# Optimization experiments

Hardware: AMD Instinct MI355X
Metric: run time of the kernel (lower is better)

## Reference

```python
import jax, jax.numpy as jnp
import numpy as np

B, T, C, N = 2, 2048, 4096, 4096

def setup_inputs() -> dict:
    key = jax.random.key(0)
    k1, k2, k3, k4 = jax.random.split(key, 4)
    y = jax.random.normal(k1, (B, T, C), dtype=jnp.float32)
    # quantized weight: uint8 codes in [0,255], stored/used as float after upcast
    weight = jnp.round(jax.random.uniform(k2, (C, N), dtype=jnp.float32) * 255.0)
    rng = jax.random.uniform(k3, (1, 1, C), dtype=jnp.float32) * 0.01  # per-input-channel scale
    offset = jax.random.normal(k4, (C,), dtype=jnp.float32) * 0.01    # per-input-channel offset
    return {"y": y, "weight": weight, "rng": rng, "offset": offset}

def reference(y, weight, rng, offset):
    # yv = y.reshape(-1,C) @ offset -> [B,T,1] correction term
    yv = jnp.einsum('btc,c->bt', y, offset)[..., None]
    # (y * range) @ weight  (dequantized GEMM) + correction
    out = jnp.einsum('btc,cn->btn', y * rng, weight) + yv
    return out
```

## Files before the change

### kernel.cpp

```cpp
#include <hip/hip_runtime.h>

typedef unsigned short u16;
typedef unsigned int u32;
typedef unsigned char u8;
typedef signed char i8;

typedef int i32x4 __attribute__((ext_vector_type(4)));

__global__ __launch_bounds__(256) void quant_y_kernel(const float* __restrict__ y,
                                                      const float* __restrict__ rng,
                                                      const float* __restrict__ off,
                                                      uint4* __restrict__ qy,
                                                      float* __restrict__ sp,
                                                      float* __restrict__ tv) {
    const int row = blockIdx.x;
    const int tid = threadIdx.x;
    const float* yr = y + (size_t)row * 4096;
    const int base = tid * 16;

    float ysr[16];
    float amax = 0.0f, s1 = 0.0f, s2 = 0.0f;
    #pragma unroll
    for (int ii = 0; ii < 4; ++ii) {
        float4 v = *(const float4*)&yr[base + ii * 4];
        float4 g = *(const float4*)&rng[base + ii * 4];
        float4 o = *(const float4*)&off[base + ii * 4];
        float p0 = v.x * g.x, p1 = v.y * g.y, p2 = v.z * g.z, p3 = v.w * g.w;
        ysr[ii * 4 + 0] = p0; ysr[ii * 4 + 1] = p1;
        ysr[ii * 4 + 2] = p2; ysr[ii * 4 + 3] = p3;
        s1 += p0 + p1 + p2 + p3;
        s2 += v.x * o.x + v.y * o.y + v.z * o.z + v.w * o.w;
        amax = fmaxf(amax, fmaxf(fmaxf(fabsf(p0), fabsf(p1)), fmaxf(fabsf(p2), fabsf(p3))));
    }
    #pragma unroll
    for (int d = 32; d > 0; d >>= 1) {
        amax = fmaxf(amax, __shfl_down(amax, d));
        s1 += __shfl_down(s1, d);
        s2 += __shfl_down(s2, d);
    }
    __shared__ float ra[4], rs1[4], rs2[4];
    const int wv = tid >> 6;
    if ((tid & 63) == 0) { ra[wv] = amax; rs1[wv] = s1; rs2[wv] = s2; }
    __syncthreads();
    const float sm = fmaxf(fmaxf(ra[0], ra[1]), fmaxf(ra[2], ra[3]));
    const float inv = sm > 0.0f ? 127.0f / sm : 0.0f;

    u32 d[4];
    #pragma unroll
    for (int g = 0; g < 4; ++g) {
        u32 b0 = (u8)(i8)(int)rintf(ysr[g * 4 + 0] * inv);
        u32 b1 = (u8)(i8)(int)rintf(ysr[g * 4 + 1] * inv);
        u32 b2 = (u8)(i8)(int)rintf(ysr[g * 4 + 2] * inv);
        u32 b3 = (u8)(i8)(int)rintf(ysr[g * 4 + 3] * inv);
        d[g] = b0 | (b1 << 8) | (b2 << 16) | (b3 << 24);
    }
    const int j = (tid & 7) ^ (row & 7);
    qy[(size_t)row * 256 + (tid >> 3) * 8 + j] = make_uint4(d[0], d[1], d[2], d[3]);
    if (tid == 0) {
        sp[row] = sm / 127.0f;
        tv[row] = 128.0f * (rs1[0] + rs1[1] + rs1[2] + rs1[3])
                        + (rs2[0] + rs2[1] + rs2[2] + rs2[3]);
    }
}

__global__ __launch_bounds__(256) void quant_w_kernel(const float* __restrict__ w,
                                                      uint4* __restrict__ wq) {
    __shared__ i8 tile[64][68];
    const int n0 = (blockIdx.x & 63) * 64;
    const int k0 = (blockIdx.x >> 6) * 64;
    const int c4 = threadIdx.x & 15;
    const int r0 = threadIdx.x >> 4;
    #pragma unroll
    for (int i = 0; i < 4; ++i) {
        int kk = r0 + i * 16;
        float4 v = *(const float4*)&w[(size_t)(k0 + kk) * 4096 + n0 + c4 * 4];
        u32 b0 = (u8)(i8)((int)v.x - 128);
        u32 b1 = (u8)(i8)((int)v.y - 128);
        u32 b2 = (u8)(i8)((int)v.z - 128);
        u32 b3 = (u8)(i8)((int)v.w - 128);
        *(u32*)&tile[kk][c4 * 4] = b0 | (b1 << 8) | (b2 << 16) | (b3 << 24);
    }
    __syncthreads();
    const int nl = threadIdx.x >> 2;
    const int ci = threadIdx.x & 3;
    const int l = ((k0 >> 4) & 7) + ci;
    const int j = l ^ ((n0 + nl) & 7);
    u32 d[4];
    #pragma unroll
    for (int g = 0; g < 4; ++g) {
        int kl = ci * 16 + g * 4;
        d[g] = (u32)(u8)tile[kl + 0][nl] | ((u32)(u8)tile[kl + 1][nl] << 8)
             | ((u32)(u8)tile[kl + 2][nl] << 16) | ((u32)(u8)tile[kl + 3][nl] << 24);
    }
    wq[(size_t)(n0 + nl) * 256 + (k0 >> 7) * 8 + j] = make_uint4(d[0], d[1], d[2], d[3]);
}

__device__ inline void gld16(const i8* g, i8* l) {
    __builtin_amdgcn_global_load_lds((const __attribute__((address_space(1))) void*)g,
                                     (__attribute__((address_space(3))) void*)l,
                                     16, 0, 0);
}

__global__ __launch_bounds__(256) void gemm_kernel(const i8* __restrict__ qy,
                                                   const i8* __restrict__ wq,
                                                   const float* __restrict__ sp,
                                                   const float* __restrict__ tv,
                                                   float* __restrict__ out) {
    __shared__ i8 As[128 * 128];
    __shared__ i8 Bs[128 * 128];
    const int bid = blockIdx.x;
    const int xcd = bid & 7;
    const int jj = bid >> 3;
    const int bn = (xcd * 4 + (jj & 3)) * 128;
    const int bm = (jj >> 2) * 128;

    const int lane = threadIdx.x & 63;
    const int wv = threadIdx.x >> 6;
    const int wm = (wv >> 1) * 64;
    const int wn = (wv & 1) * 64;
    const int r = lane & 15;
    const int q = lane >> 4;
    const int j0 = q ^ (r & 7);

    const int rsub = lane >> 3;
    const int jsub = lane & 7;
    const i8* gA[4]; const i8* gB[4]; i8* lA[4]; i8* lB[4];
    #pragma unroll
    for (int c = 0; c < 4; ++c) {
        int ca = wv * 4 + c;
        gA[c] = qy + (size_t)(bm + ca * 8 + rsub) * 4096 + jsub * 16;
        gB[c] = wq + (size_t)(bn + ca * 8 + rsub) * 4096 + jsub * 16;
        lA[c] = &As[ca * 1024];
        lB[c] = &Bs[ca * 1024];
    }

    i32x4 acc[4][4] = {};

    for (int kt = 0; kt < 32; ++kt) {
        #pragma unroll
        for (int c = 0; c < 4; ++c) {
            gld16(gA[c], lA[c]);
            gld16(gB[c], lB[c]);
            gA[c] += 128; gB[c] += 128;
        }
        __syncthreads();

        #pragma unroll
        for (int s = 0; s < 2; ++s) {
            const int js = (j0 ^ (s * 4)) * 16;
            i32x4 af[4], bfr[4];
            #pragma unroll
            for (int i = 0; i < 4; ++i)
                af[i] = *(const i32x4*)&As[(wm + i * 16 + r) * 128 + js];
            #pragma unroll
            for (int i = 0; i < 4; ++i)
                bfr[i] = *(const i32x4*)&Bs[(wn + i * 16 + r) * 128 + js];
            #pragma unroll
            for (int i = 0; i < 4; ++i) {
                #pragma unroll
                for (int j = 0; j < 4; ++j)
                    acc[i][j] = __builtin_amdgcn_mfma_i32_16x16x64_i8(af[i], bfr[j], acc[i][j], 0, 0, 0);
            }
        }
        __syncthreads();
    }

    #pragma unroll
    for (int i = 0; i < 4; ++i) {
        #pragma unroll
        for (int rr = 0; rr < 4; ++rr) {
            const int gm = bm + wm + i * 16 + q * 4 + rr;
            const float sc = sp[gm];
            const float tt = tv[gm];
            #pragma unroll
            for (int j = 0; j < 4; ++j) {
                const int gn = bn + wn + j * 16 + r;
                out[(size_t)gm * 4096 + gn] = sc * (float)acc[i][j][rr] + tt;
            }
        }
    }
}

extern "C" void kernel_launch(void* const* d_in, const int* in_sizes, int n_in,
                              void* d_out, int out_size, void* d_ws, size_t ws_size,
                              hipStream_t stream) {
    const float* y   = (const float*)d_in[0];
    const float* w   = (const float*)d_in[1];
    const float* rng = (const float*)d_in[2];
    const float* off = (const float*)d_in[3];
    float* out = (float*)d_out;

    i8* qy = (i8*)d_ws;
    i8* wq = qy + (size_t)4096 * 4096;
    float* sp = (float*)(wq + (size_t)4096 * 4096);
    float* tv = sp + 4096;

    quant_y_kernel<<<4096, 256, 0, stream>>>(y, rng, off, (uint4*)qy, sp, tv);
    quant_w_kernel<<<4096, 256, 0, stream>>>(w, (uint4*)wq);
    gemm_kernel<<<1024, 256, 0, stream>>>(qy, wq, sp, tv, out);
}
```

Baseline: 246.7 us.

## Fuse quant kernels and use double-buffered 256x256 int8 GEMM tiles

Merges the activation and weight quantization kernels into one launch with a branch on block index. The GEMM moves to 256x256 block tiles with 8 waves, each computing 128x64. LDS is double-buffered so the next K tile's global-to-LDS loads are issued during the current tile's MFMAs, with barriers interleaved and s_setprio raised around MFMA bursts. This aims to hide load latency and raise reuse per byte, at the cost of 128KB of LDS per block and only 256 blocks, which may leave some CUs idle.

```diff
diff --git a/kernel.cpp b/kernel.cpp
--- a/kernel.cpp
+++ b/kernel.cpp
@@ -7,175 +7,235 @@
 
 typedef int i32x4 __attribute__((ext_vector_type(4)));
 
-__global__ __launch_bounds__(256) void quant_y_kernel(const float* __restrict__ y,
-                                                      const float* __restrict__ rng,
-                                                      const float* __restrict__ off,
-                                                      uint4* __restrict__ qy,
-                                                      float* __restrict__ sp,
-                                                      float* __restrict__ tv) {
-    const int row = blockIdx.x;
-    const int tid = threadIdx.x;
-    const float* yr = y + (size_t)row * 4096;
-    const int base = tid * 16;
-
-    float ysr[16];
-    float amax = 0.0f, s1 = 0.0f, s2 = 0.0f;
-    #pragma unroll
-    for (int ii = 0; ii < 4; ++ii) {
-        float4 v = *(const float4*)&yr[base + ii * 4];
-        float4 g = *(const float4*)&rng[base + ii * 4];
-        float4 o = *(const float4*)&off[base + ii * 4];
-        float p0 = v.x * g.x, p1 = v.y * g.y, p2 = v.z * g.z, p3 = v.w * g.w;
-        ysr[ii * 4 + 0] = p0; ysr[ii * 4 + 1] = p1;
-        ysr[ii * 4 + 2] = p2; ysr[ii * 4 + 3] = p3;
-        s1 += p0 + p1 + p2 + p3;
-        s2 += v.x * o.x + v.y * o.y + v.z * o.z + v.w * o.w;
-        amax = fmaxf(amax, fmaxf(fmaxf(fabsf(p0), fabsf(p1)), fmaxf(fabsf(p2), fabsf(p3))));
-    }
-    #pragma unroll
-    for (int d = 32; d > 0; d >>= 1) {
-        amax = fmaxf(amax, __shfl_down(amax, d));
-        s1 += __shfl_down(s1, d);
-        s2 += __shfl_down(s2, d);
-    }
-    __shared__ float ra[4], rs1[4], rs2[4];
-    const int wv = tid >> 6;
-    if ((tid & 63) == 0) { ra[wv] = amax; rs1[wv] = s1; rs2[wv] = s2; }
-    __syncthreads();
-    const float sm = fmaxf(fmaxf(ra[0], ra[1]), fmaxf(ra[2], ra[3]));
-    const float inv = sm > 0.0f ? 127.0f / sm : 0.0f;
-
-    u32 d[4];
-    #pragma unroll
-    for (int g = 0; g < 4; ++g) {
-        u32 b0 = (u8)(i8)(int)rintf(ysr[g * 4 + 0] * inv);
-        u32 b1 = (u8)(i8)(int)rintf(ysr[g * 4 + 1] * inv);
-        u32 b2 = (u8)(i8)(int)rintf(ysr[g * 4 + 2] * inv);
-        u32 b3 = (u8)(i8)(int)rintf(ysr[g * 4 + 3] * inv);
-        d[g] = b0 | (b1 << 8) | (b2 << 16) | (b3 << 24);
-    }
-    const int j = (tid & 7) ^ (row & 7);
-    qy[(size_t)row * 256 + (tid >> 3) * 8 + j] = make_uint4(d[0], d[1], d[2], d[3]);
-    if (tid == 0) {
-        sp[row] = sm / 127.0f;
-        tv[row] = 128.0f * (rs1[0] + rs1[1] + rs1[2] + rs1[3])
-                        + (rs2[0] + rs2[1] + rs2[2] + rs2[3]);
-    }
-}
-
-__global__ __launch_bounds__(256) void quant_w_kernel(const float* __restrict__ w,
-                                                      uint4* __restrict__ wq) {
-    __shared__ i8 tile[64][68];
-    const int n0 = (blockIdx.x & 63) * 64;
-    const int k0 = (blockIdx.x >> 6) * 64;
-    const int c4 = threadIdx.x & 15;
-    const int r0 = threadIdx.x >> 4;
-    #pragma unroll
-    for (int i = 0; i < 4; ++i) {
-        int kk = r0 + i * 16;
-        float4 v = *(const float4*)&w[(size_t)(k0 + kk) * 4096 + n0 + c4 * 4];
-        u32 b0 = (u8)(i8)((int)v.x - 128);
-        u32 b1 = (u8)(i8)((int)v.y - 128);
-        u32 b2 = (u8)(i8)((int)v.z - 128);
-        u32 b3 = (u8)(i8)((int)v.w - 128);
-        *(u32*)&tile[kk][c4 * 4] = b0 | (b1 << 8) | (b2 << 16) | (b3 << 24);
-    }
-    __syncthreads();
-    const int nl = threadIdx.x >> 2;
-    const int ci = threadIdx.x & 3;
-    const int l = ((k0 >> 4) & 7) + ci;
-    const int j = l ^ ((n0 + nl) & 7);
-    u32 d[4];
-    #pragma unroll
-    for (int g = 0; g < 4; ++g) {
-        int kl = ci * 16 + g * 4;
-        d[g] = (u32)(u8)tile[kl + 0][nl] | ((u32)(u8)tile[kl + 1][nl] << 8)
-             | ((u32)(u8)tile[kl + 2][nl] << 16) | ((u32)(u8)tile[kl + 3][nl] << 24);
-    }
-    wq[(size_t)(n0 + nl) * 256 + (k0 >> 7) * 8 + j] = make_uint4(d[0], d[1], d[2], d[3]);
-}
-
 __device__ inline void gld16(const i8* g, i8* l) {
     __builtin_amdgcn_global_load_lds((const __attribute__((address_space(1))) void*)g,
                                      (__attribute__((address_space(3))) void*)l,
                                      16, 0, 0);
 }
 
-__global__ __launch_bounds__(256) void gemm_kernel(const i8* __restrict__ qy,
-                                                   const i8* __restrict__ wq,
-                                                   const float* __restrict__ sp,
-                                                   const float* __restrict__ tv,
-                                                   float* __restrict__ out) {
-    __shared__ i8 As[128 * 128];
-    __shared__ i8 Bs[128 * 128];
+__global__ __launch_bounds__(256) void prep_kernel(const float* __restrict__ y,
+                                                   const float* __restrict__ rng,
+                                                   const float* __restrict__ off,
+                                                   const float* __restrict__ w,
+                                                   uint4* __restrict__ qy,
+                                                   uint4* __restrict__ wq,
+                                                   float* __restrict__ sp,
+                                                   float* __restrict__ tv) {
+    __shared__ i8 tile[64][68];
+    __shared__ float ra[4], rs1[4], rs2[4];
+    const int tid = threadIdx.x;
+
+    if (blockIdx.x < 4096) {
+        const int row = blockIdx.x;
+        const float* yr = y + (size_t)row * 4096;
+        const int base = tid * 16;
+
+        float ysr[16];
+        float amax = 0.0f, s1 = 0.0f, s2 = 0.0f;
+        #pragma unroll
+        for (int ii = 0; ii < 4; ++ii) {
+            float4 v = *(const float4*)&yr[base + ii * 4];
+            float4 g = *(const float4*)&rng[base + ii * 4];
+            float4 o = *(const float4*)&off[base + ii * 4];
+            float p0 = v.x * g.x, p1 = v.y * g.y, p2 = v.z * g.z, p3 = v.w * g.w;
+            ysr[ii * 4 + 0] = p0; ysr[ii * 4 + 1] = p1;
+            ysr[ii * 4 + 2] = p2; ysr[ii * 4 + 3] = p3;
+            s1 += p0 + p1 + p2 + p3;
+            s2 += v.x * o.x + v.y * o.y + v.z * o.z + v.w * o.w;
+            amax = fmaxf(amax, fmaxf(fmaxf(fabsf(p0), fabsf(p1)), fmaxf(fabsf(p2), fabsf(p3))));
+        }
+        #pragma unroll
+        for (int d = 32; d > 0; d >>= 1) {
+            amax = fmaxf(amax, __shfl_down(amax, d));
+            s1 += __shfl_down(s1, d);
+            s2 += __shfl_down(s2, d);
+        }
+        const int wv = tid >> 6;
+        if ((tid & 63) == 0) { ra[wv] = amax; rs1[wv] = s1; rs2[wv] = s2; }
+        __syncthreads();
+        const float sm = fmaxf(fmaxf(ra[0], ra[1]), fmaxf(ra[2], ra[3]));
+        const float inv = sm > 0.0f ? 127.0f / sm : 0.0f;
+
+        u32 d[4];
+        #pragma unroll
+        for (int g = 0; g < 4; ++g) {
+            u32 b0 = (u8)(i8)(int)rintf(ysr[g * 4 + 0] * inv);
+            u32 b1 = (u8)(i8)(int)rintf(ysr[g * 4 + 1] * inv);
+            u32 b2 = (u8)(i8)(int)rintf(ysr[g * 4 + 2] * inv);
+            u32 b3 = (u8)(i8)(int)rintf(ysr[g * 4 + 3] * inv);
+            d[g] = b0 | (b1 << 8) | (b2 << 16) | (b3 << 24);
+        }
+        const int j = (tid & 7) ^ (row & 7);
+        qy[(size_t)row * 256 + (tid >> 3) * 8 + j] = make_uint4(d[0], d[1], d[2], d[3]);
+        if (tid == 0) {
+            sp[row] = sm / 127.0f;
+            tv[row] = 128.0f * (rs1[0] + rs1[1] + rs1[2] + rs1[3])
+                            + (rs2[0] + rs2[1] + rs2[2] + rs2[3]);
+        }
+    } else {
+        const int bid = blockIdx.x - 4096;
+        const int n0 = (bid & 63) * 64;
+        const int k0 = (bid >> 6) * 64;
+        const int c4 = tid & 15;
+        const int r0 = tid >> 4;
+        #pragma unroll
+        for (int i = 0; i < 4; ++i) {
+            int kk = r0 + i * 16;
+            float4 v = *(const float4*)&w[(size_t)(k0 + kk) * 4096 + n0 + c4 * 4];
+            u32 b0 = (u8)(i8)((int)v.x - 128);
+            u32 b1 = (u8)(i8)((int)v.y - 128);
+            u32 b2 = (u8)(i8)((int)v.z - 128);
+            u32 b3 = (u8)(i8)((int)v.w - 128);
+            *(u32*)&tile[kk][c4 * 4] = b0 | (b1 << 8) | (b2 << 16) | (b3 << 24);
+        }
+        __syncthreads();
+        const int nl = tid >> 2;
+        const int ci = tid & 3;
+        const int l = ((k0 >> 4) & 7) + ci;
+        const int j = l ^ ((n0 + nl) & 7);
+        u32 d[4];
+        #pragma unroll
+        for (int g = 0; g < 4; ++g) {
+            int kl = ci * 16 + g * 4;
+            d[g] = (u32)(u8)tile[kl + 0][nl] | ((u32)(u8)tile[kl + 1][nl] << 8)
+                 | ((u32)(u8)tile[kl + 2][nl] << 16) | ((u32)(u8)tile[kl + 3][nl] << 24);
+        }
+        wq[(size_t)(n0 + nl) * 256 + (k0 >> 7) * 8 + j] = make_uint4(d[0], d[1], d[2], d[3]);
+    }
+}
+
+__global__ __launch_bounds__(512, 2) void gemm_kernel(const i8* __restrict__ qy,
+                                                      const i8* __restrict__ wq,
+                                                      const float* __restrict__ sp,
+                                                      const float* __restrict__ tv,
+                                                      float* __restrict__ out) {
+    __shared__ i8 As[2][256 * 128];
+    __shared__ i8 Bs[2][256 * 128];
+
     const int bid = blockIdx.x;
     const int xcd = bid & 7;
     const int jj = bid >> 3;
-    const int bn = (xcd * 4 + (jj & 3)) * 128;
-    const int bm = (jj >> 2) * 128;
-
-    const int lane = threadIdx.x & 63;
-    const int wv = threadIdx.x >> 6;
-    const int wm = (wv >> 1) * 64;
-    const int wn = (wv & 1) * 64;
+    const int bn = (xcd * 2 + (jj & 1)) * 256;
+    const int bm = (jj >> 1) * 256;
+
+    const int tid = (int)threadIdx.x;
+    const int lane = tid & 63;
+    const int wv = tid >> 6;
+    const int wm = (wv >> 2) * 128;
+    const int wn = (wv & 3) * 64;
     const int r = lane & 15;
     const int q = lane >> 4;
-    const int j0 = q ^ (r & 7);
+    const int col0 = (q ^ (r & 7)) << 4;
+
+    const int offA0 = (wm + r) * 128 + col0;
+    const int offB0 = (wn + r) * 128 + col0;
+    const int offA1 = offA0 ^ 64;
+    const int offB1 = offB0 ^ 64;
 
     const int rsub = lane >> 3;
     const int jsub = lane & 7;
-    const i8* gA[4]; const i8* gB[4]; i8* lA[4]; i8* lB[4];
+    const i8* gA[4]; const i8* gB[4];
+    int ldso[4];
     #pragma unroll
     for (int c = 0; c < 4; ++c) {
-        int ca = wv * 4 + c;
+        const int ca = wv * 4 + c;
         gA[c] = qy + (size_t)(bm + ca * 8 + rsub) * 4096 + jsub * 16;
         gB[c] = wq + (size_t)(bn + ca * 8 + rsub) * 4096 + jsub * 16;
-        lA[c] = &As[ca * 1024];
-        lB[c] = &Bs[ca * 1024];
-    }
-
-    i32x4 acc[4][4] = {};
-
-    for (int kt = 0; kt < 32; ++kt) {
-        #pragma unroll
-        for (int c = 0; c < 4; ++c) {
-            gld16(gA[c], lA[c]);
-            gld16(gB[c], lB[c]);
-            gA[c] += 128; gB[c] += 128;
-        }
-        __syncthreads();
-
-        #pragma unroll
-        for (int s = 0; s < 2; ++s) {
-            const int js = (j0 ^ (s * 4)) * 16;
-            i32x4 af[4], bfr[4];
-            #pragma unroll
-            for (int i = 0; i < 4; ++i)
-                af[i] = *(const i32x4*)&As[(wm + i * 16 + r) * 128 + js];
-            #pragma unroll
-            for (int i = 0; i < 4; ++i)
-                bfr[i] = *(const i32x4*)&Bs[(wn + i * 16 + r) * 128 + js];
-            #pragma unroll
-            for (int i = 0; i < 4; ++i) {
-                #pragma unroll
-                for (int j = 0; j < 4; ++j)
-                    acc[i][j] = __builtin_amdgcn_mfma_i32_16x16x64_i8(af[i], bfr[j], acc[i][j], 0, 0, 0);
-            }
-        }
-        __syncthreads();
-    }
-
-    #pragma unroll
-    for (int i = 0; i < 4; ++i) {
+        ldso[c] = ca * 1024;
+    }
+
+    i32x4 acc[8][4] = {};
+    i32x4 a[4][2], b[4][2];
+
+    #pragma unroll
+    for (int c = 0; c < 4; ++c) { gld16(gA[c], &As[0][ldso[c]]); gA[c] += 128; }
+    #pragma unroll
+    for (int c = 0; c < 4; ++c) { gld16(gB[c], &Bs[0][ldso[c]]); gB[c] += 128; }
+    asm volatile("s_waitcnt vmcnt(0)" ::: "memory");
+    __builtin_amdgcn_s_barrier();
+
+#define RD_A4(RB, MB)                                                         \
+    _Pragma("unroll")                                                         \
+    for (int mi = 0; mi < 4; ++mi) {                                          \
+        a[mi][0] = *(const i32x4*)&As[RB][offA0 + (MB + mi) * 2048];          \
+        a[mi][1] = *(const i32x4*)&As[RB][offA1 + (MB + mi) * 2048];          \
+    }
+#define RD_B2(RB, NB)                                                         \
+    _Pragma("unroll")                                                         \
+    for (int ni = 0; ni < 2; ++ni) {                                          \
+        b[NB + ni][0] = *(const i32x4*)&Bs[RB][offB0 + (NB + ni) * 2048];     \
+        b[NB + ni][1] = *(const i32x4*)&Bs[RB][offB1 + (NB + ni) * 2048];     \
+    }
+#define MM16(MB, NB)                                                          \
+    _Pragma("unroll")                                                         \
+    for (int mi = 0; mi < 4; ++mi) {                                          \
+        _Pragma("unroll")                                                     \
+        for (int ni = 0; ni < 2; ++ni) {                                      \
+            acc[MB + mi][NB + ni] = __builtin_amdgcn_mfma_i32_16x16x64_i8(    \
+                a[mi][0], b[NB + ni][0], acc[MB + mi][NB + ni], 0, 0, 0);     \
+            acc[MB + mi][NB + ni] = __builtin_amdgcn_mfma_i32_16x16x64_i8(    \
+                a[mi][1], b[NB + ni][1], acc[MB + mi][NB + ni], 0, 0, 0);     \
+        }                                                                     \
+    }
+#define WAIT_LGKM do { asm volatile("s_waitcnt lgkmcnt(0)" ::: "memory");     \
+                       __builtin_amdgcn_sched_barrier(0); } while (0)
+
+#define KTILE(RB, WB, PF)                                                     \
+    do {                                                                      \
+                                                  \
+        RD_A4(RB, 0); RD_B2(RB, 0);                                           \
+        if (PF) {                                                             \
+            _Pragma("unroll")                                                 \
+            for (int c = 0; c < 4; ++c) { gld16(gA[c], &As[WB][ldso[c]]); gA[c] += 128; } \
+        }                                                                     \
+        __builtin_amdgcn_s_barrier(); WAIT_LGKM;                              \
+        __builtin_amdgcn_s_setprio(1); MM16(0, 0); __builtin_amdgcn_s_setprio(0); \
+        __builtin_amdgcn_s_barrier();                                         \
+                                                            \
+        RD_B2(RB, 2);                                                         \
+        if (PF) {                                                             \
+            _Pragma("unroll")                                                 \
+            for (int c = 0; c < 4; ++c) { gld16(gB[c], &Bs[WB][ldso[c]]); gB[c] += 128; } \
+        }                                                                     \
+        __builtin_amdgcn_s_barrier(); WAIT_LGKM;                              \
+        __builtin_amdgcn_s_setprio(1); MM16(0, 2); __builtin_amdgcn_s_setprio(0); \
+        __builtin_amdgcn_s_barrier();                                         \
+                                  \
+        RD_A4(RB, 4);                                                         \
+        __builtin_amdgcn_s_barrier(); WAIT_LGKM;                              \
+        __builtin_amdgcn_s_setprio(1); MM16(4, 0); __builtin_amdgcn_s_setprio(0); \
+        __builtin_amdgcn_s_barrier();                                         \
+                  \
+        __builtin_amdgcn_s_setprio(1); MM16(4, 2); __builtin_amdgcn_s_setprio(0); \
+        asm volatile("s_waitcnt vmcnt(0)" ::: "memory");                      \
+        __builtin_amdgcn_s_barrier();                                         \
+    } while (0)
+
+    #pragma unroll 1
+    for (int t = 0; t < 15; ++t) {
+        KTILE(0, 1, 1);
+        KTILE(1, 0, 1);
+    }
+    KTILE(0, 1, 1);
+    KTILE(1, 0, 0);
+
+#undef KTILE
+#undef WAIT_LGKM
+#undef MM16
+#undef RD_B2
+#undef RD_A4
+
+    #pragma unroll
+    for (int mi = 0; mi < 8; ++mi) {
         #pragma unroll
         for (int rr = 0; rr < 4; ++rr) {
-            const int gm = bm + wm + i * 16 + q * 4 + rr;
+            const int gm = bm + wm + mi * 16 + q * 4 + rr;
             const float sc = sp[gm];
             const float tt = tv[gm];
             #pragma unroll
-            for (int j = 0; j < 4; ++j) {
-                const int gn = bn + wn + j * 16 + r;
-                out[(size_t)gm * 4096 + gn] = sc * (float)acc[i][j][rr] + tt;
+            for (int ni = 0; ni < 4; ++ni) {
+                const int gn = bn + wn + ni * 16 + r;
+                out[(size_t)gm * 4096 + gn] = sc * (float)acc[mi][ni][rr] + tt;
             }
         }
     }
@@ -195,7 +255,6 @@
     float* sp = (float*)(wq + (size_t)4096 * 4096);
     float* tv = sp + 4096;
 
-    quant_y_kernel<<<4096, 256, 0, stream>>>(y, rng, off, (uint4*)qy, sp, tv);
-    quant_w_kernel<<<4096, 256, 0, stream>>>(w, (uint4*)wq);
-    gemm_kernel<<<1024, 256, 0, stream>>>(qy, wq, sp, tv, out);
-}
+    prep_kernel<<<8192, 256, 0, stream>>>(y, rng, off, w, (uint4*)qy, (uint4*)wq, sp, tv);
+    gemm_kernel<<<256, 512, 0, stream>>>(qy, wq, sp, tv, out);
+}
```

Result: faster. 239.9 us (-2.8%).
